# Optimization experiments

Hardware: AMD Instinct MI355X
Metric: run time of the kernel (lower is better)

The kernel has to match this reference:

```python
import jax, jax.numpy as jnp
import numpy as np

OBS_DIM = 512
BACKBONE_DIMS = [1024, 1024, 512]
EXPERT_HIDDEN = 256
NUM_EXPERTS = 16
NUM_ACTIONS = 32
BATCH = 65536


def _glorot(key, shape):
    fan_in = shape[-2] if len(shape) >= 2 else shape[-1]
    return jax.random.normal(key, shape, dtype=jnp.float32) * (1.0 / np.sqrt(fan_in))


def setup_inputs() -> dict:
    key = jax.random.key(0)
    ks = jax.random.split(key, 16)
    inp = {}
    inp['obs'] = jax.random.normal(ks[0], (BATCH, OBS_DIM), dtype=jnp.float32)
    # shared backbone: 512->1024->1024->512 (Linear+ReLU+Dropout(eval=identity))
    dims = [OBS_DIM] + BACKBONE_DIMS
    for i in range(3):
        inp[f'Wb{i}'] = _glorot(ks[1 + i], (dims[i], dims[i + 1]))
        inp[f'bb{i}'] = jnp.zeros((dims[i + 1],), dtype=jnp.float32)
    # experts, batched over expert dim: 512->256->ReLU->256->32
    inp['We1'] = _glorot(ks[4], (NUM_EXPERTS, BACKBONE_DIMS[-1], EXPERT_HIDDEN))
    inp['be1'] = jnp.zeros((NUM_EXPERTS, EXPERT_HIDDEN), dtype=jnp.float32)
    inp['We2'] = _glorot(ks[5], (NUM_EXPERTS, EXPERT_HIDDEN, NUM_ACTIONS))
    inp['be2'] = jnp.zeros((NUM_EXPERTS, NUM_ACTIONS), dtype=jnp.float32)
    # motion selector: 512->256->128->16 + softmax
    inp['Ws0'] = _glorot(ks[6], (OBS_DIM, 256))
    inp['bs0'] = jnp.zeros((256,), dtype=jnp.float32)
    inp['Ws1'] = _glorot(ks[7], (256, 128))
    inp['bs1'] = jnp.zeros((128,), dtype=jnp.float32)
    inp['Ws2'] = _glorot(ks[8], (128, NUM_EXPERTS))
    inp['bs2'] = jnp.zeros((NUM_EXPERTS,), dtype=jnp.float32)
    return inp


def reference(obs, Wb0, bb0, Wb1, bb1, Wb2, bb2, We1, be1, We2, be2,
              Ws0, bs0, Ws1, bs1, Ws2, bs2):
    # shared backbone (Dropout is identity in eval/inference)
    h = jax.nn.relu(obs @ Wb0 + bb0)
    h = jax.nn.relu(h @ Wb1 + bb1)
    h = jax.nn.relu(h @ Wb2 + bb2)  # [B, 512]
    # all experts on shared features, as one batched GEMM
    eh = jax.nn.relu(jnp.einsum('bd,edh->beh', h, We1) + be1)       # [B, E, 256]
    expert_actions = jnp.einsum('beh,eha->bea', eh, We2) + be2       # [B, E, A]
    # motion selector (softmax fusion weights)
    s = jax.nn.relu(obs @ Ws0 + bs0)
    s = jax.nn.relu(s @ Ws1 + bs1)
    w = jax.nn.softmax(s @ Ws2 + bs2, axis=-1)                        # [B, E]
    # softmax-weighted fusion over experts
    fused = jnp.einsum('bea,be->ba', expert_actions, w)              # [B, A]
    return fused
```

## Files before the change

### kernel.cpp

```cpp
#include <hip/hip_runtime.h>
#include <hip/hip_bf16.h>
#include <stdint.h>

typedef __attribute__((ext_vector_type(8))) short short8;
typedef __attribute__((ext_vector_type(4))) float f32x4;

__device__ __forceinline__ float b2f(short s) {
    union { unsigned u; float f; } v; v.u = ((unsigned)(unsigned short)s) << 16; return v.f;
}
__device__ __forceinline__ short f2b(float f) {
    union { float f; unsigned u; } v; v.f = f;
    unsigned r = (v.u + 0x7FFF + ((v.u >> 16) & 1)) >> 16;
    return (short)r;
}

__device__ __forceinline__ void gload16(const void* g, void* l) {
    __builtin_amdgcn_global_load_lds(
        (const __attribute__((address_space(1))) void*)(uintptr_t)g,
        (__attribute__((address_space(3))) void*)(uintptr_t)l,
        16, 0, 0);
}

#define BAR()     asm volatile("s_barrier" ::: "memory")
#define WAITV0()  asm volatile("s_waitcnt vmcnt(0)" ::: "memory")

__global__ __launch_bounds__(256) void cast_bf16_kernel(
    const float* __restrict__ src, short* __restrict__ dst, int n8) {
    int i = blockIdx.x * 256 + threadIdx.x;
    if (i >= n8) return;
    const float4* s = (const float4*)src + (size_t)i * 2;
    float4 x0 = s[0], x1 = s[1];
    short8 o;
    o[0] = f2b(x0.x); o[1] = f2b(x0.y); o[2] = f2b(x0.z); o[3] = f2b(x0.w);
    o[4] = f2b(x1.x); o[5] = f2b(x1.y); o[6] = f2b(x1.z); o[7] = f2b(x1.w);
    *((short8*)dst + i) = o;
}

__global__ __launch_bounds__(256) void transpose_cast_kernel(
    const float* __restrict__ W, short* __restrict__ Wt, int K, int N, int total) {
    int t = blockIdx.x * 256 + threadIdx.x;
    if (t >= total) return;
    const float* src = W + (size_t)blockIdx.y * K * N;
    short* dst = Wt + (size_t)blockIdx.y * K * N;
    int n = t % N;
    int k0 = (t / N) * 8;
    short8 o;
#pragma unroll
    for (int i = 0; i < 8; i++) o[i] = f2b(src[(size_t)(k0 + i) * N + n]);
    *(short8*)(dst + (size_t)n * K + k0) = o;
}

__global__ __launch_bounds__(256, 3)
void sel_fused(const short* __restrict__ s0, const short* __restrict__ Ws1t,
               const float* __restrict__ bs1, const short* __restrict__ Ws2t,
               const float* __restrict__ bs2, float* __restrict__ wsel) {
    __shared__ __align__(16) short As[128 * 32];
    __shared__ __align__(16) short Bs[128 * 32];
    __shared__ __align__(16) short s1l[128 * 136];
    const int tid = threadIdx.x;
    const int w = tid >> 6, lane = tid & 63;
    const int tm = blockIdx.x * 128;
    const int wm = (w & 1) * 64, wn = (w >> 1) * 64;
    const int r = lane & 15, q = lane >> 4, qk = q * 8;

    const int c0 = w * 2, c1 = w * 2 + 1;
    const int srow0 = c0 * 16 + (lane >> 2);
    const int srow1 = c1 * 16 + (lane >> 2);
    const int skk = (lane & 3) * 8;
    const short* gA0 = s0 + (size_t)(tm + srow0) * 256 + skk;
    const short* gA1 = s0 + (size_t)(tm + srow1) * 256 + skk;
    const short* gB0 = Ws1t + (size_t)srow0 * 256 + skk;
    const short* gB1 = Ws1t + (size_t)srow1 * 256 + skk;
    short* lA0 = &As[c0 * 512]; short* lA1 = &As[c1 * 512];
    short* lB0 = &Bs[c0 * 512]; short* lB1 = &Bs[c1 * 512];

    f32x4 acc[4][4] = {};
    for (int k0 = 0; k0 < 256; k0 += 32) {
        gload16(gA0 + k0, lA0);
        gload16(gA1 + k0, lA1);
        gload16(gB0 + k0, lB0);
        gload16(gB1 + k0, lB1);
        __syncthreads();
        short8 a[4], b[4];
#pragma unroll
        for (int i = 0; i < 4; i++) a[i] = *(const short8*)&As[(wm + i * 16 + r) * 32 + qk];
#pragma unroll
        for (int j = 0; j < 4; j++) b[j] = *(const short8*)&Bs[(wn + j * 16 + r) * 32 + qk];
#pragma unroll
        for (int i = 0; i < 4; i++)
#pragma unroll
            for (int j = 0; j < 4; j++)
                acc[i][j] = __builtin_amdgcn_mfma_f32_16x16x32_bf16(a[i], b[j], acc[i][j], 0, 0, 0);
        __syncthreads();
    }
#pragma unroll
    for (int j = 0; j < 4; j++) {
        int col = wn + j * 16 + r;
        float bj = bs1[col];
#pragma unroll
        for (int i = 0; i < 4; i++)
#pragma unroll
            for (int rr = 0; rr < 4; rr++) {
                int row = wm + i * 16 + q * 4 + rr;
                s1l[row * 136 + col] = f2b(fmaxf(acc[i][j][rr] + bj, 0.f));
            }
    }
    __syncthreads();
    f32x4 acc3[2] = {};
#pragma unroll
    for (int k3 = 0; k3 < 4; ++k3) {
        short8 b3 = *(const short8*)(Ws2t + (size_t)r * 128 + k3 * 32 + qk);
#pragma unroll
        for (int m2 = 0; m2 < 2; m2++) {
            short8 a3 = *(const short8*)&s1l[(w * 32 + m2 * 16 + r) * 136 + k3 * 32 + qk];
            acc3[m2] = __builtin_amdgcn_mfma_f32_16x16x32_bf16(a3, b3, acc3[m2], 0, 0, 0);
        }
    }
    float bse = bs2[r];
#pragma unroll
    for (int m2 = 0; m2 < 2; m2++)
#pragma unroll
        for (int rr = 0; rr < 4; rr++) {
            int row = tm + w * 32 + m2 * 16 + q * 4 + rr;
            float v = acc3[m2][rr] + bse;
            float m = v;
#pragma unroll
            for (int off = 8; off >= 1; off >>= 1) m = fmaxf(m, __shfl_xor(m, off, 16));
            float ex = __expf(v - m);
            float s = ex;
#pragma unroll
            for (int off = 8; off >= 1; off >>= 1) s += __shfl_xor(s, off, 16);
            wsel[(size_t)row * 16 + r] = ex / s;
        }
}

__global__ __launch_bounds__(256)
void reduce_kernel(const float* __restrict__ partial, const float* __restrict__ wsel,
                   const float* __restrict__ be2, float* __restrict__ out) {
    int t = blockIdx.x * 256 + threadIdx.x;
    int a4 = t & 7, i = t >> 3;
    int by = i >> 8, r = i & 255;
    const float* p = partial + (size_t)by * 16 * 8192 + r * 32 + a4 * 4;
    const float* wr = wsel + (size_t)i * 16;
    f32x4 s = {};
#pragma unroll
    for (int e = 0; e < 16; e++) {
        float wv = wr[e];
        const float* b2 = be2 + e * 32 + a4 * 4;
#pragma unroll
        for (int j = 0; j < 4; j++) s[j] = fmaf(wv, b2[j], s[j]);
    }
#pragma unroll
    for (int bx = 0; bx < 16; bx++) s += *(const f32x4*)(p + (size_t)bx * 8192);
    *(f32x4*)(out + (size_t)i * 32 + a4 * 4) = s;
}

template<int MODE>
__global__ __launch_bounds__(512, 2)
void gemm256(const short* __restrict__ A, const short* __restrict__ Bt,
             const float* __restrict__ bias, const float* __restrict__ wselp,
             const short* __restrict__ W2, short* __restrict__ C,
             float* __restrict__ pout, const float* __restrict__ bias2,
             short* __restrict__ C2, int M, int N, int K) {
    extern __shared__ __align__(16) short lds[];
    const int tid = threadIdx.x;
    const int w = tid >> 6, lane = tid & 63;
    const int wr = w >> 2, wc = w & 3;

    const int gx = gridDim.x;
    const int b = blockIdx.y * gx + blockIdx.x;
    int bx, by;
    {
        const int per = (gx * gridDim.y) >> 3;
        const int sb = (b & 7) * per + (b >> 3);
        bx = sb % gx; by = sb / gx;
    }
    const int tm = by * 256, tn = bx * 256;

    const int rih = w * 8 + (lane >> 3);
    const int colel = (((lane & 7) ^ (lane >> 3)) << 3);
    const short* pA = A + (size_t)(tm + rih) * K + colel;
    const short* pB = Bt + (size_t)(tn + rih) * K + colel;
    const size_t rK64 = (size_t)64 * K, rK128 = (size_t)128 * K;
    short* const ldsw = lds + w * 512;

#define STG_A(buf, h, t) do { \
        const short* s_ = pA + (size_t)(h) * rK128 + (size_t)(t) * 64; \
        short* d_ = ldsw + (buf) * 32768 + (h) * 8192; \
        gload16(s_, d_); \
        gload16(s_ + rK64, d_ + 4096); } while (0)
#define STG_B(buf, h, t) do { \
        const short* s_ = pB + (size_t)(h) * rK128 + (size_t)(t) * 64; \
        short* d_ = ldsw + (buf) * 32768 + 16384 + (h) * 8192; \
        gload16(s_, d_); \
        gload16(s_ + rK64, d_ + 4096); } while (0)

    const int rA = lane & 15, q = lane >> 4;
    const int csw0 = ((q << 4)) ^ ((lane & 7) << 4);
    const int csw1 = (64 + (q << 4)) ^ ((lane & 7) << 4);
    const char* const ldsB_ = (const char*)lds;
    const int aBase0 = wr * 16384 + rA * 128;
    const int bBase0 = 32768 + (wc >> 1) * 16384 + ((wc & 1) * 64 + rA) * 128;

    f32x4 acc[8][4] = {};
    short8 aL[4][2], aH[4][2], b0[2][2], b1[2][2];
    const int nt = K >> 6;

    STG_A(0, 0, 0); STG_A(0, 1, 0); STG_B(0, 0, 0); STG_B(0, 1, 0);
    WAITV0(); BAR();
    {
        const char* pa = ldsB_ + aBase0;
        const char* pb = ldsB_ + bBase0;
#pragma unroll
        for (int m = 0; m < 4; m++) {
            aL[m][0] = *(const short8*)(pa + m * 2048 + csw0);
            aL[m][1] = *(const short8*)(pa + m * 2048 + csw1);
        }
#pragma unroll
        for (int n = 0; n < 2; n++) {
            b0[n][0] = *(const short8*)(pb + n * 2048 + csw0);
            b0[n][1] = *(const short8*)(pb + n * 2048 + csw1);
        }
    }

    for (int t = 0; t < nt; ++t) {
        const int cur = t & 1, nxt = cur ^ 1;
        const char* pa = ldsB_ + cur * 65536 + aBase0;
        const char* pb = ldsB_ + cur * 65536 + bBase0;
#pragma unroll
        for (int n = 0; n < 2; n++) {
            b1[n][0] = *(const short8*)(pb + (2 + n) * 2048 + csw0);
            b1[n][1] = *(const short8*)(pb + (2 + n) * 2048 + csw1);
        }
        if (t + 1 < nt) {
            STG_A(nxt, 0, t + 1); STG_A(nxt, 1, t + 1);
            STG_B(nxt, 0, t + 1); STG_B(nxt, 1, t + 1);
        }
        __builtin_amdgcn_s_setprio(1);
#pragma unroll
        for (int m = 0; m < 4; m++)
#pragma unroll
            for (int n = 0; n < 2; n++) {
                acc[m][n] = __builtin_amdgcn_mfma_f32_16x16x32_bf16(aL[m][0], b0[n][0], acc[m][n], 0, 0, 0);
                acc[m][n] = __builtin_amdgcn_mfma_f32_16x16x32_bf16(aL[m][1], b0[n][1], acc[m][n], 0, 0, 0);
            }
        __builtin_amdgcn_s_setprio(0);
#pragma unroll
        for (int m = 0; m < 4; m++) {
            aH[m][0] = *(const short8*)(pa + (4 + m) * 2048 + csw0);
            aH[m][1] = *(const short8*)(pa + (4 + m) * 2048 + csw1);
        }
        __builtin_amdgcn_s_setprio(1);
#pragma unroll
        for (int m = 0; m < 4; m++)
#pragma unroll
            for (int n = 0; n < 2; n++) {
                acc[m][2 + n] = __builtin_amdgcn_mfma_f32_16x16x32_bf16(aL[m][0], b1[n][0], acc[m][2 + n], 0, 0, 0);
                acc[m][2 + n] = __builtin_amdgcn_mfma_f32_16x16x32_bf16(aL[m][1], b1[n][1], acc[m][2 + n], 0, 0, 0);
            }
        __builtin_amdgcn_s_setprio(0);
        __builtin_amdgcn_s_setprio(1);
#pragma unroll
        for (int m = 0; m < 4; m++)
#pragma unroll
            for (int n = 0; n < 2; n++) {
                acc[4 + m][2 + n] = __builtin_amdgcn_mfma_f32_16x16x32_bf16(aH[m][0], b1[n][0], acc[4 + m][2 + n], 0, 0, 0);
                acc[4 + m][2 + n] = __builtin_amdgcn_mfma_f32_16x16x32_bf16(aH[m][1], b1[n][1], acc[4 + m][2 + n], 0, 0, 0);
            }
        __builtin_amdgcn_s_setprio(0);
        __builtin_amdgcn_s_setprio(1);
#pragma unroll
        for (int m = 0; m < 4; m++)
#pragma unroll
            for (int n = 0; n < 2; n++) {
                acc[4 + m][n] = __builtin_amdgcn_mfma_f32_16x16x32_bf16(aH[m][0], b0[n][0], acc[4 + m][n], 0, 0, 0);
                acc[4 + m][n] = __builtin_amdgcn_mfma_f32_16x16x32_bf16(aH[m][1], b0[n][1], acc[4 + m][n], 0, 0, 0);
            }
        __builtin_amdgcn_s_setprio(0);
        WAITV0(); BAR();
        if (t + 1 < nt) {
            const char* qa = ldsB_ + nxt * 65536 + aBase0;
            const char* qb = ldsB_ + nxt * 65536 + bBase0;
#pragma unroll
            for (int m = 0; m < 4; m++) {
                aL[m][0] = *(const short8*)(qa + m * 2048 + csw0);
                aL[m][1] = *(const short8*)(qa + m * 2048 + csw1);
            }
#pragma unroll
            for (int n = 0; n < 2; n++) {
                b0[n][0] = *(const short8*)(qb + n * 2048 + csw0);
                b0[n][1] = *(const short8*)(qb + n * 2048 + csw1);
            }
        }
    }
#undef STG_A
#undef STG_B

    const int q4 = q * 4;
    float biasv[4];
#pragma unroll
    for (int n = 0; n < 4; n++) {
        const int col = tn + wc * 64 + n * 16 + rA;
        biasv[n] = (MODE == 3 && tn >= 1024) ? bias2[col - 1024] : bias[col];
    }

    if (MODE == 2) {
        const int e = tn >> 8;
        char* ldsc = (char*)lds;
#pragma unroll
        for (int m = 0; m < 8; m++)
#pragma unroll
            for (int rr = 0; rr < 4; rr++) {
                const int row = wr * 128 + m * 16 + q4 + rr;
                const float ws = wselp[(size_t)(tm + row) * 16 + e];
#pragma unroll
                for (int n = 0; n < 4; n++) {
                    const int col = wc * 64 + n * 16 + rA;
                    const float v = fmaxf(acc[m][n][rr] + biasv[n], 0.f) * ws;
                    *(short*)(ldsc + row * 512 + ((col * 2) ^ ((row & 7) << 4))) = f2b(v);
                }
            }
        asm volatile("s_waitcnt lgkmcnt(0)" ::: "memory");
        BAR();
        f32x4 g2[2][2] = {};
#pragma unroll
        for (int k2 = 0; k2 < 8; ++k2) {
            short8 a2[2], b2[2];
#pragma unroll
            for (int m2 = 0; m2 < 2; m2++) {
                const int row = w * 32 + m2 * 16 + rA;
                a2[m2] = *(const short8*)(ldsc + row * 512 + ((k2 * 64 + q * 16) ^ ((row & 7) << 4)));
            }
#pragma unroll
            for (int n2 = 0; n2 < 2; n2++)
                b2[n2] = *(const short8*)(W2 + (size_t)(e * 32 + n2 * 16 + rA) * 256 + k2 * 32 + q * 8);
#pragma unroll
            for (int m2 = 0; m2 < 2; m2++)
#pragma unroll
                for (int n2 = 0; n2 < 2; n2++)
                    g2[m2][n2] = __builtin_amdgcn_mfma_f32_16x16x32_bf16(a2[m2], b2[n2], g2[m2][n2], 0, 0, 0);
        }
        float* pp = pout + ((size_t)(tm >> 8) * 16 + e) * 8192;
#pragma unroll
        for (int m2 = 0; m2 < 2; m2++)
#pragma unroll
            for (int rr = 0; rr < 4; rr++) {
                const int row = w * 32 + m2 * 16 + q4 + rr;
#pragma unroll
                for (int n2 = 0; n2 < 2; n2++)
                    pp[row * 32 + n2 * 16 + rA] = g2[m2][n2][rr];
            }
        return;
    }

#pragma unroll
    for (int m = 0; m < 8; m++)
#pragma unroll
        for (int rr = 0; rr < 4; rr++) {
            const int row = tm + wr * 128 + m * 16 + q4 + rr;
#pragma unroll
            for (int n = 0; n < 4; n++) {
                const int col = tn + wc * 64 + n * 16 + rA;
                float v = fmaxf(acc[m][n][rr] + biasv[n], 0.f);
                if (MODE == 3 && tn >= 1024)
                    C2[(size_t)row * 256 + (col - 1024)] = f2b(v);
                else
                    C[(size_t)row * N + col] = f2b(v);
            }
        }
}

extern "C" void kernel_launch(void* const* d_in, const int* in_sizes, int n_in,
                              void* d_out, int out_size, void* d_ws, size_t ws_size,
                              hipStream_t stream) {
    const float* obs = (const float*)d_in[0];
    const float* Wb0 = (const float*)d_in[1]; const float* bb0 = (const float*)d_in[2];
    const float* Wb1 = (const float*)d_in[3]; const float* bb1 = (const float*)d_in[4];
    const float* Wb2 = (const float*)d_in[5]; const float* bb2 = (const float*)d_in[6];
    const float* We1 = (const float*)d_in[7]; const float* be1 = (const float*)d_in[8];
    const float* We2 = (const float*)d_in[9]; const float* be2 = (const float*)d_in[10];
    const float* Ws0 = (const float*)d_in[11]; const float* bs0 = (const float*)d_in[12];
    const float* Ws1 = (const float*)d_in[13]; const float* bs1 = (const float*)d_in[14];
    const float* Ws2 = (const float*)d_in[15]; const float* bs2 = (const float*)d_in[16];

    const int B = 65536;
    char* ws = (char*)d_ws;
    size_t off = 0;
    auto alloc = [&](size_t bytes) { void* p = ws + off; off += (bytes + 255) & ~(size_t)255; return p; };
    short* obs_bf = (short*)alloc((size_t)B * 512 * 2);
    short* h1     = (short*)alloc((size_t)B * 1024 * 2);
    short* h2     = (short*)alloc((size_t)B * 1024 * 2);
    short* hbuf   = (short*)alloc((size_t)B * 512 * 2);
    short* s0     = (short*)alloc((size_t)B * 256 * 2);
    float* wsel   = (float*)alloc((size_t)B * 16 * 4);
    short* WbS0t  = (short*)alloc((size_t)1280 * 512 * 2);
    short* Wb1t   = (short*)alloc((size_t)1024 * 1024 * 2);
    short* Wb2t   = (short*)alloc((size_t)1024 * 512 * 2);
    short* We1t   = (short*)alloc((size_t)16 * 512 * 256 * 2);
    short* We2t   = (short*)alloc((size_t)16 * 256 * 32 * 2);
    short* Ws1t   = (short*)alloc((size_t)256 * 128 * 2);
    short* Ws2t   = (short*)alloc((size_t)128 * 16 * 2);
    float* partial = (float*)h1;

    static int inited = 0;
    if (!inited) {
        hipFuncSetAttribute(reinterpret_cast<const void*>(gemm256<0>),
                            hipFuncAttributeMaxDynamicSharedMemorySize, 131072);
        hipFuncSetAttribute(reinterpret_cast<const void*>(gemm256<2>),
                            hipFuncAttributeMaxDynamicSharedMemorySize, 131072);
        hipFuncSetAttribute(reinterpret_cast<const void*>(gemm256<3>),
                            hipFuncAttributeMaxDynamicSharedMemorySize, 131072);
        inited = 1;
    }

    cast_bf16_kernel<<<(B * 512 / 8 + 255) / 256, 256, 0, stream>>>(obs, obs_bf, B * 512 / 8);
    transpose_cast_kernel<<<dim3((1024 * 512 / 8 + 255) / 256, 1), 256, 0, stream>>>(Wb0, WbS0t, 512, 1024, 1024 * 512 / 8);
    transpose_cast_kernel<<<dim3((256 * 512 / 8 + 255) / 256, 1), 256, 0, stream>>>(Ws0, WbS0t + (size_t)1024 * 512, 512, 256, 256 * 512 / 8);
    transpose_cast_kernel<<<dim3((1024 * 1024 / 8 + 255) / 256, 1), 256, 0, stream>>>(Wb1, Wb1t, 1024, 1024, 1024 * 1024 / 8);
    transpose_cast_kernel<<<dim3((512 * 1024 / 8 + 255) / 256, 1), 256, 0, stream>>>(Wb2, Wb2t, 1024, 512, 512 * 1024 / 8);
    transpose_cast_kernel<<<dim3((256 * 512 / 8 + 255) / 256, 16), 256, 0, stream>>>(We1, We1t, 512, 256, 256 * 512 / 8);
    transpose_cast_kernel<<<dim3((32 * 256 / 8 + 255) / 256, 16), 256, 0, stream>>>(We2, We2t, 256, 32, 32 * 256 / 8);
    transpose_cast_kernel<<<dim3((128 * 256 / 8 + 255) / 256, 1), 256, 0, stream>>>(Ws1, Ws1t, 256, 128, 128 * 256 / 8);
    transpose_cast_kernel<<<dim3((16 * 128 / 8 + 255) / 256, 1), 256, 0, stream>>>(Ws2, Ws2t, 128, 16, 16 * 128 / 8);

    gemm256<3><<<dim3(5, B / 256), 512, 131072, stream>>>(
        obs_bf, WbS0t, bb0, nullptr, nullptr, h1, nullptr, bs0, s0, B, 1024, 512);
    sel_fused<<<B / 128, 256, 0, stream>>>(s0, Ws1t, bs1, Ws2t, bs2, wsel);

    gemm256<0><<<dim3(4, B / 256), 512, 131072, stream>>>(
        h1, Wb1t, bb1, nullptr, nullptr, h2, nullptr, nullptr, nullptr, B, 1024, 1024);
    gemm256<0><<<dim3(2, B / 256), 512, 131072, stream>>>(
        h2, Wb2t, bb2, nullptr, nullptr, hbuf, nullptr, nullptr, nullptr, B, 512, 1024);

    gemm256<2><<<dim3(16, B / 256), 512, 131072, stream>>>(
        hbuf, We1t, be1, wsel, We2t, nullptr, partial, nullptr, nullptr, B, 4096, 512);
    reduce_kernel<<<B * 8 / 256, 256, 0, stream>>>(partial, wsel, be2, (float*)d_out);
}
```

Before: 980.2 us.

## Replace 256-tile backbone GEMMs with simple 128x128 single-buffered MFMA kernel

```diff
diff --git a/kernel.cpp b/kernel.cpp
--- a/kernel.cpp
+++ b/kernel.cpp
@@ -48,6 +48,68 @@
 #pragma unroll
     for (int i = 0; i < 8; i++) o[i] = f2b(src[(size_t)(k0 + i) * N + n]);
     *(short8*)(dst + (size_t)n * K + k0) = o;
+}
+
+template<int DUAL>
+__global__ __launch_bounds__(256, 3)
+void gemm_bt_bias_relu(const short* __restrict__ A, const short* __restrict__ Bt,
+                       const float* __restrict__ bias, short* __restrict__ C,
+                       const float* __restrict__ bias2, short* __restrict__ C2,
+                       int M, int N, int K) {
+    __shared__ __align__(16) short As[128 * 32];
+    __shared__ __align__(16) short Bs[128 * 32];
+    const int tid = threadIdx.x;
+    const int w = tid >> 6, lane = tid & 63;
+    const int tm = blockIdx.y * 128, tn = blockIdx.x * 128;
+    const int wm = (w & 1) * 64, wn = (w >> 1) * 64;
+    const int r = lane & 15, q = lane >> 4, qk = q * 8;
+
+    const int c0 = w * 2, c1 = w * 2 + 1;
+    const int srow0 = c0 * 16 + (lane >> 2);
+    const int srow1 = c1 * 16 + (lane >> 2);
+    const int skk = (lane & 3) * 8;
+    const short* gA0 = A + (size_t)(tm + srow0) * K + skk;
+    const short* gA1 = A + (size_t)(tm + srow1) * K + skk;
+    const short* gB0 = Bt + (size_t)(tn + srow0) * K + skk;
+    const short* gB1 = Bt + (size_t)(tn + srow1) * K + skk;
+    short* lA0 = &As[c0 * 512]; short* lA1 = &As[c1 * 512];
+    short* lB0 = &Bs[c0 * 512]; short* lB1 = &Bs[c1 * 512];
+
+    f32x4 acc[4][4] = {};
+    for (int k0 = 0; k0 < K; k0 += 32) {
+        gload16(gA0 + k0, lA0);
+        gload16(gA1 + k0, lA1);
+        gload16(gB0 + k0, lB0);
+        gload16(gB1 + k0, lB1);
+        __syncthreads();
+        short8 a[4], b[4];
+#pragma unroll
+        for (int i = 0; i < 4; i++) a[i] = *(const short8*)&As[(wm + i * 16 + r) * 32 + qk];
+#pragma unroll
+        for (int j = 0; j < 4; j++) b[j] = *(const short8*)&Bs[(wn + j * 16 + r) * 32 + qk];
+#pragma unroll
+        for (int i = 0; i < 4; i++)
+#pragma unroll
+            for (int j = 0; j < 4; j++)
+                acc[i][j] = __builtin_amdgcn_mfma_f32_16x16x32_bf16(a[i], b[j], acc[i][j], 0, 0, 0);
+        __syncthreads();
+    }
+#pragma unroll
+    for (int j = 0; j < 4; j++) {
+        int col = tn + wn + j * 16 + r;
+        float bj = (DUAL && col >= 1024) ? bias2[col - 1024] : bias[col];
+#pragma unroll
+        for (int i = 0; i < 4; i++)
+#pragma unroll
+            for (int rr = 0; rr < 4; rr++) {
+                int row = tm + wm + i * 16 + q * 4 + rr;
+                float v = fmaxf(acc[i][j][rr] + bj, 0.f);
+                if (DUAL && col >= 1024)
+                    C2[(size_t)row * 256 + (col - 1024)] = f2b(v);
+                else
+                    C[(size_t)row * N + col] = f2b(v);
+            }
+    }
 }
 
 __global__ __launch_bounds__(256, 3)
@@ -301,7 +363,7 @@
 #pragma unroll
     for (int n = 0; n < 4; n++) {
         const int col = tn + wc * 64 + n * 16 + rA;
-        biasv[n] = (MODE == 3 && tn >= 1024) ? bias2[col - 1024] : bias[col];
+        biasv[n] = bias[col];
     }
 
     if (MODE == 2) {
@@ -362,10 +424,7 @@
             for (int n = 0; n < 4; n++) {
                 const int col = tn + wc * 64 + n * 16 + rA;
                 float v = fmaxf(acc[m][n][rr] + biasv[n], 0.f);
-                if (MODE == 3 && tn >= 1024)
-                    C2[(size_t)row * 256 + (col - 1024)] = f2b(v);
-                else
-                    C[(size_t)row * N + col] = f2b(v);
+                C[(size_t)row * N + col] = f2b(v);
             }
         }
 }
@@ -404,11 +463,7 @@
 
     static int inited = 0;
     if (!inited) {
-        hipFuncSetAttribute(reinterpret_cast<const void*>(gemm256<0>),
-                            hipFuncAttributeMaxDynamicSharedMemorySize, 131072);
         hipFuncSetAttribute(reinterpret_cast<const void*>(gemm256<2>),
-                            hipFuncAttributeMaxDynamicSharedMemorySize, 131072);
-        hipFuncSetAttribute(reinterpret_cast<const void*>(gemm256<3>),
                             hipFuncAttributeMaxDynamicSharedMemorySize, 131072);
         inited = 1;
     }
@@ -423,14 +478,14 @@
     transpose_cast_kernel<<<dim3((128 * 256 / 8 + 255) / 256, 1), 256, 0, stream>>>(Ws1, Ws1t, 256, 128, 128 * 256 / 8);
     transpose_cast_kernel<<<dim3((16 * 128 / 8 + 255) / 256, 1), 256, 0, stream>>>(Ws2, Ws2t, 128, 16, 16 * 128 / 8);
 
-    gemm256<3><<<dim3(5, B / 256), 512, 131072, stream>>>(
-        obs_bf, WbS0t, bb0, nullptr, nullptr, h1, nullptr, bs0, s0, B, 1024, 512);
+    gemm_bt_bias_relu<1><<<dim3(10, B / 128), 256, 0, stream>>>(
+        obs_bf, WbS0t, bb0, h1, bs0, s0, B, 1024, 512);
     sel_fused<<<B / 128, 256, 0, stream>>>(s0, Ws1t, bs1, Ws2t, bs2, wsel);
 
-    gemm256<0><<<dim3(4, B / 256), 512, 131072, stream>>>(
-        h1, Wb1t, bb1, nullptr, nullptr, h2, nullptr, nullptr, nullptr, B, 1024, 1024);
-    gemm256<0><<<dim3(2, B / 256), 512, 131072, stream>>>(
-        h2, Wb2t, bb2, nullptr, nullptr, hbuf, nullptr, nullptr, nullptr, B, 512, 1024);
+    gemm_bt_bias_relu<0><<<dim3(8, B / 128), 256, 0, stream>>>(
+        h1, Wb1t, bb1, h2, nullptr, nullptr, B, 1024, 1024);
+    gemm_bt_bias_relu<0><<<dim3(4, B / 128), 256, 0, stream>>>(
+        h2, Wb2t, bb2, hbuf, nullptr, nullptr, B, 512, 1024);
 
     gemm256<2><<<dim3(16, B / 256), 512, 131072, stream>>>(
         hbuf, We1t, be1, wsel, We2t, nullptr, partial, nullptr, nullptr, B, 4096, 512);
```

After: 1.093 ms. +11.5%, slower.
